# Kernel optimization log

Hardware: AMD Instinct MI355X
Metric: run time of the kernel (lower is better)

## Reference

```python
import jax, jax.numpy as jnp
import numpy as np

D_MODEL = 256
NHEAD = 8
HEAD_DIM = D_MODEL // NHEAD
CLIP = 10.0
LN_EPS = 1e-5


def setup_inputs() -> dict:
    key = jax.random.key(0)
    ks = jax.random.split(key, 10)
    B, N, d = 2, 256, D_MODEL
    s = 1.0 / np.sqrt(d)
    return {
        "nodes": jax.random.normal(ks[0], (B, N, d), jnp.float32),
        "edges": jax.random.normal(ks[1], (B, N, N, d), jnp.float32),
        # shared projection (used for Q, K, V, edge-Q, edge-K, output)
        "W": jax.random.normal(ks[2], (d, d), jnp.float32) * s,
        "b": jax.random.normal(ks[3], (d,), jnp.float32) * 0.01,
        # shared LayerNorm params (same module applied twice)
        "ln_g": jnp.ones((d,), jnp.float32),
        "ln_b": jnp.zeros((d,), jnp.float32),
        # feedforward
        "W1": jax.random.normal(ks[4], (d, 4 * d), jnp.float32) * s,
        "b1": jnp.zeros((4 * d,), jnp.float32),
        "W2": jax.random.normal(ks[5], (4 * d, d), jnp.float32) * (1.0 / np.sqrt(4 * d)),
        "b2": jnp.zeros((d,), jnp.float32),
    }


def _layer_norm(x, g, b):
    mu = jnp.mean(x, axis=-1, keepdims=True)
    var = jnp.var(x, axis=-1, keepdims=True)
    return (x - mu) * jax.lax.rsqrt(var + LN_EPS) * g + b


def reference(nodes, edges, W, b, ln_g, ln_b, W1, b1, W2, b2):
    B, N, d = nodes.shape
    h, hd = NHEAD, HEAD_DIM

    x = _layer_norm(nodes, ln_g, ln_b)

    # Node projections (shared weight -> q == k == v)
    nq = (x @ W + b).reshape(B, N, h, hd)
    nk = nq
    nv = nq

    # Edge projections (shared weight -> eq == ek)
    eq = (edges @ W + b).reshape(B, N, N, h, hd)
    ek = eq

    # Broadcast-add node+edge queries/keys: [B, N, N, h, hd]
    query = eq + nq[:, :, None, :, :]
    key = ek + nk[:, None, :, :, :]

    scores = jnp.einsum("bijhd,bijhd->bhij", query, key) / np.sqrt(hd)
    scores = CLIP * jnp.tanh(scores)
    attn = jax.nn.softmax(scores, axis=-1)  # [B, h, N, N]

    # attn @ V: [B, h, N, hd] -> [B, N, d]
    out = jnp.einsum("bhij,bjhd->bihd", attn, nv).reshape(B, N, d)
    out = out @ W + b

    x = x + out
    x = _layer_norm(x, ln_g, ln_b)
    ff = jax.nn.gelu(x @ W1 + b1, approximate=False) @ W2 + b2
    return ff + x
```

## Files before the change

### kernel.cpp

```cpp
#include <hip/hip_runtime.h>

typedef _Float16 half_t;
typedef __attribute__((ext_vector_type(8))) _Float16 f16x8;
typedef __attribute__((ext_vector_type(4))) float f32x4;

#define DM 256
#define NH 8
#define NN 256
#define NB 2
#define JT 32
#define KC 64

__global__ __launch_bounds__(1024) void k_ln_proj(
    const float* __restrict__ nodes, const float* __restrict__ W,
    const float* __restrict__ bias, const float* __restrict__ ln_g,
    const float* __restrict__ ln_b, float* __restrict__ xs,
    float* __restrict__ nqv) {
  __shared__ float sx[2][DM];
  __shared__ float pp[4][2][DM];
  __shared__ float rs[8], rq[8];
  const int t = threadIdx.x;
  const int r0 = blockIdx.x * 2;
  const int row = t >> 8, col = t & 255;
  float v = 0.f;
  if (t < 512) v = nodes[(size_t)(r0 + row) * DM + col];
  float s = v, q = v * v;
#pragma unroll
  for (int m = 1; m <= 32; m <<= 1) {
    s += __shfl_xor(s, m, 64);
    q += __shfl_xor(q, m, 64);
  }
  if (t < 512 && (t & 63) == 0) { rs[t >> 6] = s; rq[t >> 6] = q; }
  __syncthreads();
  if (t < 512) {
    int rb = row * 4;
    float ss = rs[rb] + rs[rb + 1] + rs[rb + 2] + rs[rb + 3];
    float qq = rq[rb] + rq[rb + 1] + rq[rb + 2] + rq[rb + 3];
    float mu = ss * (1.f / DM);
    float var = qq * (1.f / DM) - mu * mu;
    float xv = (v - mu) * rsqrtf(var + 1e-5f) * ln_g[col] + ln_b[col];
    sx[row][col] = xv;
    xs[(size_t)(r0 + row) * DM + col] = xv;
  }
  __syncthreads();
  const int rg = t >> 8;
  float a0 = 0.f, a1 = 0.f;
#pragma unroll 8
  for (int kk = 0; kk < 64; ++kk) {
    int k = rg * 64 + kk;
    float wv = W[(size_t)k * DM + col];
    a0 += sx[0][k] * wv;
    a1 += sx[1][k] * wv;
  }
  pp[rg][0][col] = a0;
  pp[rg][1][col] = a1;
  __syncthreads();
  if (t < 512) {
    float r = pp[0][row][col] + pp[1][row][col] + pp[2][row][col] +
              pp[3][row][col] + bias[col];
    nqv[(size_t)(r0 + row) * DM + col] = r;
  }
}

__global__ __launch_bounds__(256) void k_wt16(const float* __restrict__ W,
                                              half_t* __restrict__ WT) {
  int c = blockIdx.x, t = threadIdx.x;
  WT[c * DM + t] = (half_t)W[t * DM + c];
}

__global__ __launch_bounds__(256, 3) void k_edge_scores(
    const float* __restrict__ edges, const half_t* __restrict__ WT,
    const float* __restrict__ xs, const float* __restrict__ bias,
    float* __restrict__ scores) {
  __shared__ __align__(16) char smem[8192];
  const int tid = threadIdx.x;
  const int l = tid & 63;
  const int w = tid >> 6;
  const int idx = blockIdx.x;
  const int jb = idx & 7;
  const int i = (idx >> 3) & (NN - 1);
  const int b = idx >> 11;
  const int j0 = jb * JT;

  f32x4 accq[4][2], acck[4][2];
#pragma unroll
  for (int ct = 0; ct < 4; ++ct) {
    f32x4 bv = *(const f32x4*)(bias + w * 64 + ct * 16 + (l >> 4) * 4);
    f32x4 iv = {2.f * bv[0], 2.f * bv[1], 2.f * bv[2], 2.f * bv[3]};
#pragma unroll
    for (int jt = 0; jt < 2; ++jt) { accq[ct][jt] = iv; acck[ct][jt] = iv; }
  }

  const float* eg = edges + ((size_t)(b * NN + i) * NN + j0) * DM;
  const float* xb = xs + (size_t)b * NN * DM;
  const float* xi = xb + (size_t)i * DM;
  const int f4 = tid & 15, row0 = tid >> 4;
  const char* wtb = (const char*)WT;

  f32x4 pe[2], pxj[2], pxi;
#pragma unroll
  for (int q = 0; q < 2; ++q) {
    int row = row0 + q * 16;
    pe[q] = *(const f32x4*)(eg + row * DM + f4 * 4);
    pxj[q] = *(const f32x4*)(xb + (size_t)(j0 + row) * DM + f4 * 4);
  }
  pxi = *(const f32x4*)(xi + f4 * 4);

  for (int kc = 0; kc < 4; ++kc) {
    f16x8 wf[2][4];
#pragma unroll
    for (int ks = 0; ks < 2; ++ks)
#pragma unroll
      for (int ct = 0; ct < 4; ++ct) {
        int c = w * 64 + ct * 16 + (l & 15);
        wf[ks][ct] = *(const f16x8*)(wtb + c * 512 + kc * 128 + ks * 64 +
                                     ((l >> 4) * 16));
      }
#pragma unroll
    for (int q = 0; q < 2; ++q) {
      int row = row0 + q * 16;
      union { unsigned long long u; half_t h[4]; } a1, a2;
#pragma unroll
      for (int z = 0; z < 4; ++z) {
        a1.h[z] = (half_t)(pe[q][z] + pxi[z]);
        a2.h[z] = (half_t)(pe[q][z] + pxj[q][z]);
      }
      int off = (row * 128 + f4 * 8) ^ ((row & 7) << 4);
      *(unsigned long long*)(smem + off) = a1.u;
      *(unsigned long long*)(smem + 4096 + off) = a2.u;
    }
    __syncthreads();
    if (kc < 3) {
#pragma unroll
      for (int q = 0; q < 2; ++q) {
        int row = row0 + q * 16;
        pe[q] = *(const f32x4*)(eg + row * DM + (kc + 1) * KC + f4 * 4);
        pxj[q] = *(const f32x4*)(xb + (size_t)(j0 + row) * DM + (kc + 1) * KC + f4 * 4);
      }
      pxi = *(const f32x4*)(xi + (kc + 1) * KC + f4 * 4);
    }
#pragma unroll
    for (int ks = 0; ks < 2; ++ks) {
      f16x8 fq[2], fk[2];
#pragma unroll
      for (int jt = 0; jt < 2; ++jt) {
        int r = jt * 16 + (l & 15);
        int off = (r * 128 + ks * 64 + ((l >> 4) * 16)) ^ ((r & 7) << 4);
        fq[jt] = *(const f16x8*)(smem + off);
        fk[jt] = *(const f16x8*)(smem + 4096 + off);
      }
#pragma unroll
      for (int ct = 0; ct < 4; ++ct)
#pragma unroll
        for (int jt = 0; jt < 2; ++jt) {
          accq[ct][jt] = __builtin_amdgcn_mfma_f32_16x16x32_f16(wf[ks][ct], fq[jt], accq[ct][jt], 0, 0, 0);
          acck[ct][jt] = __builtin_amdgcn_mfma_f32_16x16x32_f16(wf[ks][ct], fk[jt], acck[ct][jt], 0, 0, 0);
        }
    }
    __syncthreads();
  }

  const float scale = 0.17677669529663687f;
#pragma unroll
  for (int a = 0; a < 2; ++a) {
#pragma unroll
    for (int jt = 0; jt < 2; ++jt) {
      float s = 0.f;
#pragma unroll
      for (int u = 0; u < 2; ++u) {
        int ct = a * 2 + u;
#pragma unroll
        for (int rr = 0; rr < 4; ++rr) s += accq[ct][jt][rr] * acck[ct][jt][rr];
      }
      s += __shfl_xor(s, 16, 64);
      s += __shfl_xor(s, 32, 64);
      float sc = 10.0f * tanhf(s * scale);
      if (l < 16) {
        int h = w * 2 + a;
        int jg = j0 + jt * 16 + l;
        scores[(((size_t)(b * NH) + h) * NN + i) * NN + jg] = sc;
      }
    }
  }
}

__global__ __launch_bounds__(1024) void k_smax_av(const float* __restrict__ scores,
                                                  const float* __restrict__ nqv,
                                                  float* __restrict__ ao) {
  __shared__ float sp[NH * NN];
  __shared__ float pp[4 * 256];
  const int t = threadIdx.x;
  const int b = blockIdx.x >> 8, i = blockIdx.x & 255;
#pragma unroll
  for (int p = 0; p < 2; ++p) {
    int idx = p * 1024 + t;
    sp[idx] = scores[(((size_t)(b * NH) + (idx >> 8)) * NN + i) * NN + (idx & 255)];
  }
  __syncthreads();
  const int w = t >> 6, l = t & 63;
  if (w < 8) {
    f32x4 v = *(f32x4*)(sp + w * NN + l * 4);
    float m = fmaxf(fmaxf(v[0], v[1]), fmaxf(v[2], v[3]));
#pragma unroll
    for (int mm = 1; mm <= 32; mm <<= 1) m = fmaxf(m, __shfl_xor(m, mm, 64));
    v[0] = __expf(v[0] - m); v[1] = __expf(v[1] - m);
    v[2] = __expf(v[2] - m); v[3] = __expf(v[3] - m);
    float s = v[0] + v[1] + v[2] + v[3];
#pragma unroll
    for (int mm = 1; mm <= 32; mm <<= 1) s += __shfl_xor(s, mm, 64);
    float inv = 1.0f / s;
    v[0] *= inv; v[1] *= inv; v[2] *= inv; v[3] *= inv;
    *(f32x4*)(sp + w * NN + l * 4) = v;
  }
  __syncthreads();
  const int d = t & 255, jg = t >> 8, h = d >> 5;
  const float* vb = nqv + (size_t)b * NN * DM;
  float acc = 0.f;
#pragma unroll 8
  for (int jj = 0; jj < 64; ++jj) {
    int j = jg * 64 + jj;
    acc += sp[h * 256 + j] * vb[(size_t)j * DM + d];
  }
  pp[jg * 256 + d] = acc;
  __syncthreads();
  if (t < 256)
    ao[((size_t)(b * NN) + i) * DM + t] = pp[t] + pp[256 + t] + pp[512 + t] + pp[768 + t];
}

__global__ __launch_bounds__(1024) void k_gemm_res_ln(
    const float* __restrict__ ao, const float* __restrict__ W,
    const float* __restrict__ bias, const float* __restrict__ xs,
    const float* __restrict__ ln_g, const float* __restrict__ ln_b,
    float* __restrict__ ys) {
  __shared__ float sa[2][DM];
  __shared__ float pp[4][2][DM];
  __shared__ float rs[8], rq[8];
  const int t = threadIdx.x;
  const int r0 = blockIdx.x * 2;
  const int row = t >> 8, col = t & 255;
  if (t < 512) sa[row][col] = ao[(size_t)(r0 + row) * DM + col];
  __syncthreads();
  const int rg = t >> 8;
  float a0 = 0.f, a1 = 0.f;
#pragma unroll 8
  for (int kk = 0; kk < 64; ++kk) {
    int k = rg * 64 + kk;
    float wv = W[(size_t)k * DM + col];
    a0 += sa[0][k] * wv;
    a1 += sa[1][k] * wv;
  }
  pp[rg][0][col] = a0;
  pp[rg][1][col] = a1;
  __syncthreads();
  float val = 0.f;
  if (t < 512) {
    val = pp[0][row][col] + pp[1][row][col] + pp[2][row][col] +
          pp[3][row][col] + bias[col] + xs[(size_t)(r0 + row) * DM + col];
  }
  float s = val, q = val * val;
#pragma unroll
  for (int m = 1; m <= 32; m <<= 1) {
    s += __shfl_xor(s, m, 64);
    q += __shfl_xor(q, m, 64);
  }
  if (t < 512 && (t & 63) == 0) { rs[t >> 6] = s; rq[t >> 6] = q; }
  __syncthreads();
  if (t < 512) {
    int rb = row * 4;
    float ss = rs[rb] + rs[rb + 1] + rs[rb + 2] + rs[rb + 3];
    float qq = rq[rb] + rq[rb + 1] + rq[rb + 2] + rq[rb + 3];
    float mu = ss * (1.f / DM);
    float var = qq * (1.f / DM) - mu * mu;
    ys[(size_t)(r0 + row) * DM + col] =
        (val - mu) * rsqrtf(var + 1e-5f) * ln_g[col] + ln_b[col];
  }
}

__global__ __launch_bounds__(1024) void k_ffn1(const float* __restrict__ ys,
                                               const float* __restrict__ W1,
                                               const float* __restrict__ b1,
                                               float* __restrict__ g) {
  __shared__ float sy[2][DM];
  const int t = threadIdx.x;
  const int r0 = blockIdx.x * 2;
  if (t < 512) sy[t >> 8][t & 255] = ys[(size_t)(r0 + (t >> 8)) * DM + (t & 255)];
  __syncthreads();
  float a0 = b1[t], a1 = a0;
#pragma unroll 8
  for (int k = 0; k < DM; ++k) {
    float wv = W1[(size_t)k * 1024 + t];
    a0 += sy[0][k] * wv;
    a1 += sy[1][k] * wv;
  }
  g[(size_t)r0 * 1024 + t] = 0.5f * a0 * (1.0f + erff(a0 * 0.70710678118654752f));
  g[(size_t)(r0 + 1) * 1024 + t] = 0.5f * a1 * (1.0f + erff(a1 * 0.70710678118654752f));
}

__global__ __launch_bounds__(1024) void k_ffn2(const float* __restrict__ g,
                                               const float* __restrict__ W2,
                                               const float* __restrict__ b2,
                                               const float* __restrict__ ys,
                                               float* __restrict__ out) {
  __shared__ float sg[2][1024];
  __shared__ float pp[4][2][256];
  const int t = threadIdx.x;
  const int r0 = blockIdx.x * 2;
  if (t < 512) ((f32x4*)sg)[t] = *(const f32x4*)(g + (size_t)r0 * 1024 + t * 4);
  __syncthreads();
  const int kg = t >> 8, col = t & 255;
  float a0 = 0.f, a1 = 0.f;
#pragma unroll 8
  for (int kk = 0; kk < 256; ++kk) {
    int k = kg * 256 + kk;
    float wv = W2[(size_t)k * 256 + col];
    a0 += sg[0][k] * wv;
    a1 += sg[1][k] * wv;
  }
  pp[kg][0][col] = a0;
  pp[kg][1][col] = a1;
  __syncthreads();
  if (t < 512) {
    int row = t >> 8;
    float r = pp[0][row][col] + pp[1][row][col] + pp[2][row][col] +
              pp[3][row][col] + b2[col] + ys[(size_t)(r0 + row) * DM + col];
    out[(size_t)(r0 + row) * DM + col] = r;
  }
}

extern "C" void kernel_launch(void* const* d_in, const int* in_sizes, int n_in,
                              void* d_out, int out_size, void* d_ws, size_t ws_size,
                              hipStream_t stream) {
  const float* nodes = (const float*)d_in[0];
  const float* edges = (const float*)d_in[1];
  const float* W     = (const float*)d_in[2];
  const float* bias  = (const float*)d_in[3];
  const float* ln_g  = (const float*)d_in[4];
  const float* ln_b  = (const float*)d_in[5];
  const float* W1    = (const float*)d_in[6];
  const float* b1    = (const float*)d_in[7];
  const float* W2    = (const float*)d_in[8];
  const float* b2    = (const float*)d_in[9];
  float* out = (float*)d_out;

  char* ws = (char*)d_ws;
  float*  xs     = (float*)(ws + 0x000000);
  float*  nqv    = (float*)(ws + 0x080000);
  half_t* WT16   = (half_t*)(ws + 0x100000);
  float*  scores = (float*)(ws + 0x120000);
  float*  g      = (float*)(ws + 0x120000);
  float*  ao     = (float*)(ws + 0x520000);
  float*  ys     = (float*)(ws + 0x5A0000);

  k_ln_proj<<<NB * NN / 2, 1024, 0, stream>>>(nodes, W, bias, ln_g, ln_b, xs, nqv);
  k_wt16<<<DM, 256, 0, stream>>>(W, WT16);
  k_edge_scores<<<NB * NN * (NN / JT), 256, 0, stream>>>(edges, WT16, xs, bias, scores);
  k_smax_av<<<NB * NN, 1024, 0, stream>>>(scores, nqv, ao);
  k_gemm_res_ln<<<NB * NN / 2, 1024, 0, stream>>>(ao, W, bias, xs, ln_g, ln_b, ys);
  k_ffn1<<<NB * NN / 2, 1024, 0, stream>>>(ys, W1, b1, g);
  k_ffn2<<<NB * NN / 2, 1024, 0, stream>>>(g, W2, b2, ys, out);
}
```

Measured before the change: 319.2 us.

## Project edges once and add node projections linearly; fuse attention-out and FFN kernels

Because the projection is linear, the edge kernel now projects only the raw edge features once. It adds the precomputed node projections (with the extra bias folded in) in the epilogue, instead of running two separate GEMMs on edge+x_i and edge+x_j. This halves the MFMA work and the LDS staging in the dominant kernel, at the cost of a larger shared-memory tile for the key-side node rows, and it raises the occupancy hint to 4. It also fuses softmax/AV with the output projection, residual and LayerNorm, and fuses the two FFN GEMMs into one kernel, removing intermediate global round trips and launches.

After: 309.3 us. 3.1% less time.

```diff
diff --git a/kernel.cpp b/kernel.cpp
--- a/kernel.cpp
+++ b/kernel.cpp
@@ -9,13 +9,12 @@
 #define NN 256
 #define NB 2
 #define JT 32
-#define KC 64
 
 __global__ __launch_bounds__(1024) void k_ln_proj(
     const float* __restrict__ nodes, const float* __restrict__ W,
     const float* __restrict__ bias, const float* __restrict__ ln_g,
     const float* __restrict__ ln_b, float* __restrict__ xs,
-    float* __restrict__ nqv) {
+    float* __restrict__ nqv, float* __restrict__ nqvpb) {
   __shared__ float sx[2][DM];
   __shared__ float pp[4][2][DM];
   __shared__ float rs[8], rq[8];
@@ -56,9 +55,11 @@
   pp[rg][1][col] = a1;
   __syncthreads();
   if (t < 512) {
+    float bb = bias[col];
     float r = pp[0][row][col] + pp[1][row][col] + pp[2][row][col] +
-              pp[3][row][col] + bias[col];
+              pp[3][row][col] + bb;
     nqv[(size_t)(r0 + row) * DM + col] = r;
+    nqvpb[(size_t)(r0 + row) * DM + col] = r + bb;
   }
 }
 
@@ -68,11 +69,10 @@
   WT[c * DM + t] = (half_t)W[t * DM + c];
 }
 
-__global__ __launch_bounds__(256, 3) void k_edge_scores(
+__global__ __launch_bounds__(256, 4) void k_edge_scores(
     const float* __restrict__ edges, const half_t* __restrict__ WT,
-    const float* __restrict__ xs, const float* __restrict__ bias,
-    float* __restrict__ scores) {
-  __shared__ __align__(16) char smem[8192];
+    const float* __restrict__ nqvpb, float* __restrict__ scores) {
+  __shared__ __align__(16) char smem[4096 + 32 * 1040];
   const int tid = threadIdx.x;
   const int l = tid & 63;
   const int w = tid >> 6;
@@ -82,29 +82,30 @@
   const int b = idx >> 11;
   const int j0 = jb * JT;
 
-  f32x4 accq[4][2], acck[4][2];
-#pragma unroll
-  for (int ct = 0; ct < 4; ++ct) {
-    f32x4 bv = *(const f32x4*)(bias + w * 64 + ct * 16 + (l >> 4) * 4);
-    f32x4 iv = {2.f * bv[0], 2.f * bv[1], 2.f * bv[2], 2.f * bv[3]};
-#pragma unroll
-    for (int jt = 0; jt < 2; ++jt) { accq[ct][jt] = iv; acck[ct][jt] = iv; }
-  }
+  float* nlds = (float*)(smem + 4096);
+
+  const float* nb_ = nqvpb + ((size_t)(b * NN) + j0) * DM;
+#pragma unroll
+  for (int p = 0; p < 8; ++p) {
+    int u = p * 256 + tid;
+    int row = u >> 6, c4 = u & 63;
+    f32x4 v = *(const f32x4*)(nb_ + (size_t)row * DM + c4 * 4);
+    *(f32x4*)(nlds + row * 260 + c4 * 4) = v;
+  }
+
+  f32x4 acc[4][2];
+#pragma unroll
+  for (int ct = 0; ct < 4; ++ct)
+#pragma unroll
+    for (int jt = 0; jt < 2; ++jt) acc[ct][jt] = (f32x4){0.f, 0.f, 0.f, 0.f};
 
   const float* eg = edges + ((size_t)(b * NN + i) * NN + j0) * DM;
-  const float* xb = xs + (size_t)b * NN * DM;
-  const float* xi = xb + (size_t)i * DM;
   const int f4 = tid & 15, row0 = tid >> 4;
   const char* wtb = (const char*)WT;
 
-  f32x4 pe[2], pxj[2], pxi;
-#pragma unroll
-  for (int q = 0; q < 2; ++q) {
-    int row = row0 + q * 16;
-    pe[q] = *(const f32x4*)(eg + row * DM + f4 * 4);
-    pxj[q] = *(const f32x4*)(xb + (size_t)(j0 + row) * DM + f4 * 4);
-  }
-  pxi = *(const f32x4*)(xi + f4 * 4);
+  f32x4 pe[2];
+  pe[0] = *(const f32x4*)(eg + row0 * DM + f4 * 4);
+  pe[1] = *(const f32x4*)(eg + (row0 + 16) * DM + f4 * 4);
 
   for (int kc = 0; kc < 4; ++kc) {
     f16x8 wf[2][4];
@@ -119,62 +120,60 @@
 #pragma unroll
     for (int q = 0; q < 2; ++q) {
       int row = row0 + q * 16;
-      union { unsigned long long u; half_t h[4]; } a1, a2;
-#pragma unroll
-      for (int z = 0; z < 4; ++z) {
-        a1.h[z] = (half_t)(pe[q][z] + pxi[z]);
-        a2.h[z] = (half_t)(pe[q][z] + pxj[q][z]);
-      }
+      union { unsigned long long u; half_t h[4]; } a1;
+#pragma unroll
+      for (int z = 0; z < 4; ++z) a1.h[z] = (half_t)pe[q][z];
       int off = (row * 128 + f4 * 8) ^ ((row & 7) << 4);
       *(unsigned long long*)(smem + off) = a1.u;
-      *(unsigned long long*)(smem + 4096 + off) = a2.u;
     }
     __syncthreads();
     if (kc < 3) {
-#pragma unroll
-      for (int q = 0; q < 2; ++q) {
-        int row = row0 + q * 16;
-        pe[q] = *(const f32x4*)(eg + row * DM + (kc + 1) * KC + f4 * 4);
-        pxj[q] = *(const f32x4*)(xb + (size_t)(j0 + row) * DM + (kc + 1) * KC + f4 * 4);
-      }
-      pxi = *(const f32x4*)(xi + (kc + 1) * KC + f4 * 4);
+      pe[0] = *(const f32x4*)(eg + row0 * DM + (kc + 1) * 64 + f4 * 4);
+      pe[1] = *(const f32x4*)(eg + (row0 + 16) * DM + (kc + 1) * 64 + f4 * 4);
     }
 #pragma unroll
     for (int ks = 0; ks < 2; ++ks) {
-      f16x8 fq[2], fk[2];
+      f16x8 fq[2];
 #pragma unroll
       for (int jt = 0; jt < 2; ++jt) {
         int r = jt * 16 + (l & 15);
         int off = (r * 128 + ks * 64 + ((l >> 4) * 16)) ^ ((r & 7) << 4);
         fq[jt] = *(const f16x8*)(smem + off);
-        fk[jt] = *(const f16x8*)(smem + 4096 + off);
       }
 #pragma unroll
       for (int ct = 0; ct < 4; ++ct)
 #pragma unroll
-        for (int jt = 0; jt < 2; ++jt) {
-          accq[ct][jt] = __builtin_amdgcn_mfma_f32_16x16x32_f16(wf[ks][ct], fq[jt], accq[ct][jt], 0, 0, 0);
-          acck[ct][jt] = __builtin_amdgcn_mfma_f32_16x16x32_f16(wf[ks][ct], fk[jt], acck[ct][jt], 0, 0, 0);
-        }
+        for (int jt = 0; jt < 2; ++jt)
+          acc[ct][jt] = __builtin_amdgcn_mfma_f32_16x16x32_f16(
+              wf[ks][ct], fq[jt], acc[ct][jt], 0, 0, 0);
     }
     __syncthreads();
   }
 
+  const float* qrow = nqvpb + ((size_t)(b * NN) + i) * DM;
   const float scale = 0.17677669529663687f;
 #pragma unroll
   for (int a = 0; a < 2; ++a) {
+    float s0 = 0.f, s1 = 0.f;
+#pragma unroll
+    for (int u = 0; u < 2; ++u) {
+      int ct = a * 2 + u;
+      int cbase = w * 64 + ct * 16 + ((l >> 4) * 4);
+      f32x4 qi = *(const f32x4*)(qrow + cbase);
+      f32x4 k0 = *(const f32x4*)(nlds + (l & 15) * 260 + cbase);
+      f32x4 k1 = *(const f32x4*)(nlds + (16 + (l & 15)) * 260 + cbase);
+#pragma unroll
+      for (int rr = 0; rr < 4; ++rr) {
+        s0 += (acc[ct][0][rr] + qi[rr]) * (acc[ct][0][rr] + k0[rr]);
+        s1 += (acc[ct][1][rr] + qi[rr]) * (acc[ct][1][rr] + k1[rr]);
+      }
+    }
 #pragma unroll
     for (int jt = 0; jt < 2; ++jt) {
-      float s = 0.f;
-#pragma unroll
-      for (int u = 0; u < 2; ++u) {
-        int ct = a * 2 + u;
-#pragma unroll
-        for (int rr = 0; rr < 4; ++rr) s += accq[ct][jt][rr] * acck[ct][jt][rr];
-      }
-      s += __shfl_xor(s, 16, 64);
-      s += __shfl_xor(s, 32, 64);
-      float sc = 10.0f * tanhf(s * scale);
+      float sv = jt ? s1 : s0;
+      sv += __shfl_xor(sv, 16, 64);
+      sv += __shfl_xor(sv, 32, 64);
+      float sc = 10.0f * tanhf(sv * scale);
       if (l < 16) {
         int h = w * 2 + a;
         int jg = j0 + jt * 16 + l;
@@ -184,17 +183,21 @@
   }
 }
 
-__global__ __launch_bounds__(1024) void k_smax_av(const float* __restrict__ scores,
-                                                  const float* __restrict__ nqv,
-                                                  float* __restrict__ ao) {
+__global__ __launch_bounds__(1024) void k_attn_out(
+    const float* __restrict__ scores, const float* __restrict__ nqv,
+    const float* __restrict__ W, const float* __restrict__ bias,
+    const float* __restrict__ xs, const float* __restrict__ ln_g,
+    const float* __restrict__ ln_b, float* __restrict__ ys) {
   __shared__ float sp[NH * NN];
-  __shared__ float pp[4 * 256];
+  __shared__ float pp[4][256];
+  __shared__ float aor[256];
+  __shared__ float rs[4], rq[4];
   const int t = threadIdx.x;
   const int b = blockIdx.x >> 8, i = blockIdx.x & 255;
 #pragma unroll
   for (int p = 0; p < 2; ++p) {
-    int idx = p * 1024 + t;
-    sp[idx] = scores[(((size_t)(b * NH) + (idx >> 8)) * NN + i) * NN + (idx & 255)];
+    int idx2 = p * 1024 + t;
+    sp[idx2] = scores[(((size_t)(b * NH) + (idx2 >> 8)) * NN + i) * NN + (idx2 & 255)];
   }
   __syncthreads();
   const int w = t >> 6, l = t & 63;
@@ -213,74 +216,57 @@
     *(f32x4*)(sp + w * NN + l * 4) = v;
   }
   __syncthreads();
-  const int d = t & 255, jg = t >> 8, h = d >> 5;
+  const int d = t & 255, kg = t >> 8, h = d >> 5;
   const float* vb = nqv + (size_t)b * NN * DM;
   float acc = 0.f;
 #pragma unroll 8
   for (int jj = 0; jj < 64; ++jj) {
-    int j = jg * 64 + jj;
+    int j = kg * 64 + jj;
     acc += sp[h * 256 + j] * vb[(size_t)j * DM + d];
   }
-  pp[jg * 256 + d] = acc;
-  __syncthreads();
+  pp[kg][d] = acc;
+  __syncthreads();
+  if (t < 256) aor[t] = pp[0][t] + pp[1][t] + pp[2][t] + pp[3][t];
+  __syncthreads();
+  float a0 = 0.f;
+#pragma unroll 8
+  for (int kk = 0; kk < 64; ++kk) {
+    int k = kg * 64 + kk;
+    a0 += aor[k] * W[(size_t)k * DM + d];
+  }
+  pp[kg][d] = a0;
+  __syncthreads();
+  float val = 0.f;
   if (t < 256)
-    ao[((size_t)(b * NN) + i) * DM + t] = pp[t] + pp[256 + t] + pp[512 + t] + pp[768 + t];
-}
-
-__global__ __launch_bounds__(1024) void k_gemm_res_ln(
-    const float* __restrict__ ao, const float* __restrict__ W,
-    const float* __restrict__ bias, const float* __restrict__ xs,
-    const float* __restrict__ ln_g, const float* __restrict__ ln_b,
-    float* __restrict__ ys) {
-  __shared__ float sa[2][DM];
-  __shared__ float pp[4][2][DM];
-  __shared__ float rs[8], rq[8];
-  const int t = threadIdx.x;
-  const int r0 = blockIdx.x * 2;
-  const int row = t >> 8, col = t & 255;
-  if (t < 512) sa[row][col] = ao[(size_t)(r0 + row) * DM + col];
-  __syncthreads();
-  const int rg = t >> 8;
-  float a0 = 0.f, a1 = 0.f;
-#pragma unroll 8
-  for (int kk = 0; kk < 64; ++kk) {
-    int k = rg * 64 + kk;
-    float wv = W[(size_t)k * DM + col];
-    a0 += sa[0][k] * wv;
-    a1 += sa[1][k] * wv;
-  }
-  pp[rg][0][col] = a0;
-  pp[rg][1][col] = a1;
-  __syncthreads();
-  float val = 0.f;
-  if (t < 512) {
-    val = pp[0][row][col] + pp[1][row][col] + pp[2][row][col] +
-          pp[3][row][col] + bias[col] + xs[(size_t)(r0 + row) * DM + col];
-  }
-  float s = val, q = val * val;
+    val = pp[0][t] + pp[1][t] + pp[2][t] + pp[3][t] + bias[t] +
+          xs[((size_t)(b * NN) + i) * DM + t];
+  float s2 = val, q2 = val * val;
 #pragma unroll
   for (int m = 1; m <= 32; m <<= 1) {
-    s += __shfl_xor(s, m, 64);
-    q += __shfl_xor(q, m, 64);
-  }
-  if (t < 512 && (t & 63) == 0) { rs[t >> 6] = s; rq[t >> 6] = q; }
-  __syncthreads();
-  if (t < 512) {
-    int rb = row * 4;
-    float ss = rs[rb] + rs[rb + 1] + rs[rb + 2] + rs[rb + 3];
-    float qq = rq[rb] + rq[rb + 1] + rq[rb + 2] + rq[rb + 3];
+    s2 += __shfl_xor(s2, m, 64);
+    q2 += __shfl_xor(q2, m, 64);
+  }
+  if (t < 256 && l == 0) { rs[w] = s2; rq[w] = q2; }
+  __syncthreads();
+  if (t < 256) {
+    float ss = rs[0] + rs[1] + rs[2] + rs[3];
+    float qq = rq[0] + rq[1] + rq[2] + rq[3];
     float mu = ss * (1.f / DM);
     float var = qq * (1.f / DM) - mu * mu;
-    ys[(size_t)(r0 + row) * DM + col] =
-        (val - mu) * rsqrtf(var + 1e-5f) * ln_g[col] + ln_b[col];
-  }
-}
-
-__global__ __launch_bounds__(1024) void k_ffn1(const float* __restrict__ ys,
-                                               const float* __restrict__ W1,
-                                               const float* __restrict__ b1,
-                                               float* __restrict__ g) {
+    ys[((size_t)(b * NN) + i) * DM + t] =
+        (val - mu) * rsqrtf(var + 1e-5f) * ln_g[t] + ln_b[t];
+  }
+}
+
+__global__ __launch_bounds__(1024) void k_ffn(const float* __restrict__ ys,
+                                              const float* __restrict__ W1,
+                                              const float* __restrict__ b1,
+                                              const float* __restrict__ W2,
+                                              const float* __restrict__ b2,
+                                              float* __restrict__ out) {
   __shared__ float sy[2][DM];
+  __shared__ float sg[2][1024];
+  __shared__ float pp[4][2][256];
   const int t = threadIdx.x;
   const int r0 = blockIdx.x * 2;
   if (t < 512) sy[t >> 8][t & 255] = ys[(size_t)(r0 + (t >> 8)) * DM + (t & 255)];
@@ -292,37 +278,25 @@
     a0 += sy[0][k] * wv;
     a1 += sy[1][k] * wv;
   }
-  g[(size_t)r0 * 1024 + t] = 0.5f * a0 * (1.0f + erff(a0 * 0.70710678118654752f));
-  g[(size_t)(r0 + 1) * 1024 + t] = 0.5f * a1 * (1.0f + erff(a1 * 0.70710678118654752f));
-}
-
-__global__ __launch_bounds__(1024) void k_ffn2(const float* __restrict__ g,
-                                               const float* __restrict__ W2,
-                                               const float* __restrict__ b2,
-                                               const float* __restrict__ ys,
-                                               float* __restrict__ out) {
-  __shared__ float sg[2][1024];
-  __shared__ float pp[4][2][256];
-  const int t = threadIdx.x;
-  const int r0 = blockIdx.x * 2;
-  if (t < 512) ((f32x4*)sg)[t] = *(const f32x4*)(g + (size_t)r0 * 1024 + t * 4);
+  sg[0][t] = 0.5f * a0 * (1.0f + erff(a0 * 0.70710678118654752f));
+  sg[1][t] = 0.5f * a1 * (1.0f + erff(a1 * 0.70710678118654752f));
   __syncthreads();
   const int kg = t >> 8, col = t & 255;
-  float a0 = 0.f, a1 = 0.f;
+  float z0 = 0.f, z1 = 0.f;
 #pragma unroll 8
   for (int kk = 0; kk < 256; ++kk) {
     int k = kg * 256 + kk;
     float wv = W2[(size_t)k * 256 + col];
-    a0 += sg[0][k] * wv;
-    a1 += sg[1][k] * wv;
-  }
-  pp[kg][0][col] = a0;
-  pp[kg][1][col] = a1;
+    z0 += sg[0][k] * wv;
+    z1 += sg[1][k] * wv;
+  }
+  pp[kg][0][col] = z0;
+  pp[kg][1][col] = z1;
   __syncthreads();
   if (t < 512) {
     int row = t >> 8;
     float r = pp[0][row][col] + pp[1][row][col] + pp[2][row][col] +
-              pp[3][row][col] + b2[col] + ys[(size_t)(r0 + row) * DM + col];
+              pp[3][row][col] + b2[col] + sy[row][col];
     out[(size_t)(r0 + row) * DM + col] = r;
   }
 }
@@ -345,17 +319,14 @@
   char* ws = (char*)d_ws;
   float*  xs     = (float*)(ws + 0x000000);
   float*  nqv    = (float*)(ws + 0x080000);
-  half_t* WT16   = (half_t*)(ws + 0x100000);
-  float*  scores = (float*)(ws + 0x120000);
-  float*  g      = (float*)(ws + 0x120000);
-  float*  ao     = (float*)(ws + 0x520000);
+  float*  nqvpb  = (float*)(ws + 0x100000);
+  half_t* WT16   = (half_t*)(ws + 0x180000);
+  float*  scores = (float*)(ws + 0x1A0000);
   float*  ys     = (float*)(ws + 0x5A0000);
 
-  k_ln_proj<<<NB * NN / 2, 1024, 0, stream>>>(nodes, W, bias, ln_g, ln_b, xs, nqv);
+  k_ln_proj<<<NB * NN / 2, 1024, 0, stream>>>(nodes, W, bias, ln_g, ln_b, xs, nqv, nqvpb);
   k_wt16<<<DM, 256, 0, stream>>>(W, WT16);
-  k_edge_scores<<<NB * NN * (NN / JT), 256, 0, stream>>>(edges, WT16, xs, bias, scores);
-  k_smax_av<<<NB * NN, 1024, 0, stream>>>(scores, nqv, ao);
-  k_gemm_res_ln<<<NB * NN / 2, 1024, 0, stream>>>(ao, W, bias, xs, ln_g, ln_b, ys);
-  k_ffn1<<<NB * NN / 2, 1024, 0, stream>>>(ys, W1, b1, g);
-  k_ffn2<<<NB * NN / 2, 1024, 0, stream>>>(g, W2, b2, ys, out);
-}
+  k_edge_scores<<<NB * NN * (NN / JT), 256, 0, stream>>>(edges, WT16, nqvpb, scores);
+  k_attn_out<<<NB * NN, 1024, 0, stream>>>(scores, nqv, W, bias, xs, ln_g, ln_b, ys);
+  k_ffn<<<NB * NN / 2, 1024, 0, stream>>>(ys, W1, b1, W2, b2, out);
+}
```
